# Optimization experiments

Hardware: AMD Instinct MI355X
Metric: run time of the kernel (lower is better)

Reference implementation:

```python
import jax, jax.numpy as jnp
import numpy as np

Nc, Nt, K = 32, 64, 2
P = 1.0
BATCH = 4096
EPS_BIS = 1e-5
MAX_ITER = 100


def setup_inputs() -> dict:
    key = jax.random.key(0)
    ks = jax.random.split(key, 5)
    H = jax.random.normal(ks[0], (BATCH, K, Nc, 2 * Nt), dtype=jnp.float32)
    dims = [2 * K * K, 256, 256, 256, 4 * K]
    inp = {"H": H}
    for i in range(4):
        inp[f"W{i}"] = jax.random.normal(ks[1 + i], (dims[i], dims[i + 1]), dtype=jnp.float32) / float(np.sqrt(dims[i]))
        inp[f"b{i}"] = jnp.zeros((dims[i + 1],), dtype=jnp.float32)
    return inp


def _forward(H, W0, b0, W1, b1, W2, b2, W3, b3):
    batch = H.shape[0]
    eyeK = jnp.eye(K, dtype=jnp.complex64)
    # Source quirk: imag slice H[..., :Nt:2*Nt] has step 2*Nt>Nt -> only column 0, broadcast as imag part
    H1 = H[..., :Nt] + 1j * H[..., 0:Nt:2 * Nt]  # [b,K,Nc,Nt] complex64
    # Analog precoder: conj of center-subcarrier channel per user, unit-modulus normalized
    F_RF = jnp.conj(jnp.transpose(H1[:, :, Nc // 2, :], (0, 2, 1)))  # [b,Nt,K]
    F_RF = F_RF / jnp.abs(F_RF) / np.sqrt(Nt)
    # Source quirk: literal reshape (not permute) mixing batch and subcarrier dims
    H1r = H1.reshape(Nc, batch, K, Nt)
    H_equ = jnp.matmul(H1r, F_RF).reshape(batch, Nc, K, K)  # [Nc,b,K,Nt]@[b,Nt,K] -> [Nc,b,K,K]
    power = jnp.sum(jnp.abs(H_equ) ** 2, axis=(2, 3))  # [b,Nc]
    H_equ = H_equ / jnp.sqrt(power)[:, :, None, None]
    Hf = H_equ.reshape(batch, Nc, K * K)
    x = jnp.concatenate([jnp.real(Hf), jnp.imag(Hf)], axis=2)  # [b,Nc,2*K*K]
    # TRANS_BLOCK stand-in: MLP 8->256->256->256->4K
    for (Wl, bl, act) in ((W0, b0, True), (W1, b1, True), (W2, b2, True), (W3, b3, False)):
        x = x @ Wl + bl
        if act:
            x = jax.nn.relu(x)
    U = (x[..., 0:K] + 1j * x[..., K:2 * K]).astype(jnp.complex64)   # [b,Nc,K]
    Wm = (x[..., 2 * K:3 * K] + 1j * x[..., 3 * K:4 * K]).astype(jnp.complex64)
    Hc = H_equ.astype(jnp.complex64)  # H_hat
    coef = Wm * (jnp.abs(U) ** 2)     # [b,Nc,K]
    # B(mu) = sum_k W_k|U_k|^2 conj(h_k) h_k^T + K*mu*I  (mu*I added K times in source loop)
    B_base = jnp.einsum('bnk,bnki,bnkj->bnij', coef, jnp.conj(Hc), Hc)  # [b,Nc,K,K]
    UW = U * Wm

    def compute_V(mu, Bb, uw, hc):
        Bm = Bb + (K * mu) * eyeK
        Binv = jnp.linalg.inv(Bm)  # batched 2x2 complex inverse
        # V[:,:,i,k] = U_k W_k * (B^{-1} conj(h_k))_i
        return uw[:, :, None, :] * jnp.einsum('bnij,bnkj->bnik', Binv, jnp.conj(hc))

    # Bisection on mu for power constraint sum|V|^2 <= P
    def cond(s):
        lo, hi, mu, it = s
        return jnp.logical_and(hi - lo >= EPS_BIS, it <= MAX_ITER)

    def body(s):
        lo, hi, _, it = s
        mu = (lo + hi) / 2.0
        V = compute_V(mu, B_base, UW, Hc)
        Pitem = jnp.sum(jnp.abs(V) ** 2)
        big = Pitem > P
        return (jnp.where(big, mu, lo), jnp.where(big, hi, mu), mu, it + 1)

    init = (jnp.float32(0.0), jnp.float32(10.0), jnp.float32(5.0), jnp.int32(0))
    _, _, mu, _ = jax.lax.while_loop(cond, body, init)

    V = compute_V(mu, B_base, UW, Hc)  # [b,Nc,K,K]
    F_BB = V.reshape(Nc, batch, K, K)  # literal reshape, as in source
    F_SDMA = jnp.matmul(F_RF, F_BB).reshape(batch, Nc, Nt, K)
    Power = jnp.sum(jnp.abs(F_SDMA) ** 2, axis=(2, 3)).reshape(batch, Nc, 1, 1)
    F_BB = jnp.transpose(F_BB, (1, 0, 2, 3))
    F_BB = F_BB / jnp.sqrt(Power) * np.sqrt(K)
    F_BB = jnp.transpose(F_BB, (1, 0, 2, 3))
    F_SDMA = jnp.matmul(F_RF, F_BB)  # [Nc,b,Nt,K]
    F_SDMA = jnp.transpose(F_SDMA, (1, 0, 2, 3)).reshape(batch, K * Nc * Nt)
    return jnp.concatenate([jnp.real(F_SDMA), jnp.imag(F_SDMA)], axis=1)


def reference(H, W0, b0, W1, b1, W2, b2, W3, b3):
    return _forward(H, W0, b0, W1, b1, W2, b2, W3, b3)
```

## Files before the change

kernel.cpp:

```cpp
#include <hip/hip_runtime.h>

typedef _Float16 f16;
typedef __attribute__((ext_vector_type(8))) _Float16 f16x8;
typedef __attribute__((ext_vector_type(4))) _Float16 f16x4;
typedef __attribute__((ext_vector_type(4))) float f32x4;
typedef unsigned int u32;

#define M2N 131072
#define MFMA16 __builtin_amdgcn_mfma_f32_16x16x32_f16

struct C2 { float x, y; };
__device__ __forceinline__ C2 cmul(C2 a, C2 b){ C2 r; r.x = a.x*b.x - a.y*b.y; r.y = a.x*b.y + a.y*b.x; return r; }
__device__ __forceinline__ C2 cadd(C2 a, C2 b){ C2 r; r.x = a.x+b.x; r.y = a.y+b.y; return r; }
__device__ __forceinline__ C2 csub(C2 a, C2 b){ C2 r; r.x = a.x-b.x; r.y = a.y-b.y; return r; }
__device__ __forceinline__ C2 conjc(C2 a){ C2 r; r.x = a.x; r.y = -a.y; return r; }
__device__ __forceinline__ C2 cneg(C2 a){ C2 r; r.x = -a.x; r.y = -a.y; return r; }
__device__ __forceinline__ float cabs2(C2 a){ return a.x*a.x + a.y*a.y; }
__device__ __forceinline__ float dotr(C2 a, C2 b){ return a.x*b.x + a.y*b.y; }

__device__ __forceinline__ float wred(float v){
  #pragma unroll
  for (int s = 32; s > 0; s >>= 1) v += __shfl_xor(v, s, 64);
  return v;
}

__global__ void k_prep(const float* __restrict__ W0, const float* __restrict__ W1,
                       const float* __restrict__ W2, const float* __restrict__ W3,
                       f16* __restrict__ wfr12, f16* __restrict__ wfr0,
                       f16* __restrict__ wfr3, float* __restrict__ slots)
{
  const int b = blockIdx.x, tid = threadIdx.x;
  if (b < 64){
    const int slot = b*256 + tid;
    const int lane = slot & 63;
    const int rest = slot >> 6;
    const int kt = rest & 7, nt = (rest >> 3) & 15, L = rest >> 7;
    const float* W = L ? W2 : W1;
    const int n = nt*16 + (lane & 15);
    f16* dst = wfr12 + (size_t)rest*1024 + lane*8;
    #pragma unroll
    for (int e = 0; e < 8; ++e){
      const int k = kt*32 + (lane>>4)*8 + e;
      const float w = W[k*256 + n];
      const f16 h = (f16)w;
      dst[e] = h; dst[512+e] = (f16)(w - (float)h);
    }
  } else if (b == 64){
    for (int i = 0; i < 4; ++i){
      const int slot = i*256 + tid;
      const int lane = slot & 63, nt = slot >> 6;
      const int col = nt*16 + (lane & 15);
      f16* dst = wfr0 + (size_t)nt*1024 + lane*8;
      #pragma unroll
      for (int e = 0; e < 8; ++e){
        const int k = (lane>>4)*8 + e;
        const float w = (k < 8) ? W0[k*256 + col] : 0.f;
        const f16 h = (f16)w;
        dst[e] = h; dst[512+e] = (f16)(w - (float)h);
      }
    }
  } else {
    slots[tid] = 0.f;
    for (int i = 0; i < 2; ++i){
      const int slot = i*256 + tid;
      const int lane = slot & 63, kt = slot >> 6;
      const int col = lane & 15;
      f16* dst = wfr3 + (size_t)kt*1024 + lane*8;
      #pragma unroll
      for (int e = 0; e < 8; ++e){
        const int k = kt*32 + (lane>>4)*8 + e;
        const float w = (col < 8) ? W3[k*8 + col] : 0.f;
        const f16 h = (f16)w;
        dst[e] = h; dst[512+e] = (f16)(w - (float)h);
      }
    }
  }
}

__global__ void k_frf(const float* __restrict__ H, float2* __restrict__ frf,
                      float2* __restrict__ g2)
{
  const int b2 = blockIdx.x*2 + (threadIdx.x >> 7);
  const int tt = threadIdx.x & 127;
  const int t = tt >> 1, k = tt & 1;
  __shared__ float2 s[2][128];
  const size_t base = ((size_t)(b2*2 + k)*32 + 16)*128;
  const float are = H[base + t];
  const float aim = H[base];
  const float inv = rsqrtf(are*are + aim*aim) * 0.125f;
  float2 v; v.x = are*inv; v.y = -aim*inv;
  frf[((size_t)b2*64 + t)*2 + k] = v;
  s[threadIdx.x >> 7][tt] = v;
  __syncthreads();
  const int w = threadIdx.x >> 6;
  if ((w & 1) == 0){
    const int half = w >> 1;
    const int lane = threadIdx.x & 63;
    const float2 a = s[half][lane*2];
    const float2 b = s[half][lane*2 + 1];
    float re = a.x*b.x + a.y*b.y;
    float im = a.y*b.x - a.x*b.y;
    re = wred(re); im = wred(im);
    if (lane == 0){ float2 g; g.x = re; g.y = im; g2[blockIdx.x*2 + half] = g; }
  }
}

__global__ void k_hequ(const float* __restrict__ H, const float2* __restrict__ frf,
                       float* __restrict__ x)
{
  const int m2 = blockIdx.x*4 + (threadIdx.x >> 6);
  const int lane = threadIdx.x & 63;
  const int n = m2 >> 12, b2 = m2 & 4095;
  const float4 f = *(const float4*)(frf + ((size_t)b2*64 + lane)*2);
  float accr[2][2], acci[2][2];
  #pragma unroll
  for (int i = 0; i < 2; ++i){
    const float* hr = H + (size_t)(n*8192 + b2*2 + i) * 128;
    const float re = hr[lane];
    const float im = hr[0];
    accr[i][0] = re*f.x - im*f.y;  acci[i][0] = re*f.y + im*f.x;
    accr[i][1] = re*f.z - im*f.w;  acci[i][1] = re*f.w + im*f.z;
  }
  #pragma unroll
  for (int i = 0; i < 2; ++i)
    #pragma unroll
    for (int j = 0; j < 2; ++j){ accr[i][j] = wred(accr[i][j]); acci[i][j] = wred(acci[i][j]); }
  if (lane == 0){
    float pw = 0.f;
    #pragma unroll
    for (int i = 0; i < 2; ++i)
      #pragma unroll
      for (int j = 0; j < 2; ++j) pw += accr[i][j]*accr[i][j] + acci[i][j]*acci[i][j];
    const float rs = rsqrtf(pw);
    *(float4*)(x + (size_t)m2*8)     = make_float4(accr[0][0]*rs, accr[0][1]*rs, accr[1][0]*rs, accr[1][1]*rs);
    *(float4*)(x + (size_t)m2*8 + 4) = make_float4(acci[0][0]*rs, acci[0][1]*rs, acci[1][0]*rs, acci[1][1]*rs);
  }
}

#define SWX(r, c) ((r)*256 + ((c) ^ (((r)&7)<<3)))

__launch_bounds__(256, 3)
__global__ void k_mlp(const float* __restrict__ x, const f16* __restrict__ wfr12,
                      const f16* __restrict__ wfr0, const f16* __restrict__ wfr3,
                      const float* __restrict__ bias0, const float* __restrict__ bias1,
                      const float* __restrict__ bias2, const float* __restrict__ bias3,
                      float* __restrict__ y)
{
  __shared__ __align__(16) f16 xah[48*256];
  __shared__ __align__(16) f16 xal[48*256];
  const int tid = threadIdx.x, blk = blockIdx.x;
  const int lane = tid & 63, wv = tid >> 6;
  const int l15 = lane & 15, lh = lane >> 4;
  const int colb = wv*64;

  f32x4 acc[3][4];
  f16x8 ah[3], al[3], bh[4], bl[4];

  auto EPI = [&](){
    #pragma unroll
    for (int Mt = 0; Mt < 3; ++Mt)
      #pragma unroll
      for (int nt = 0; nt < 4; ++nt){
        f16x4 h4, l4;
        #pragma unroll
        for (int r = 0; r < 4; ++r){
          const float v = fmaxf(acc[Mt][nt][r], 0.f);
          const f16 h = (f16)v;
          h4[r] = h; l4[r] = (f16)(v - (float)h);
        }
        const int idx = SWX(Mt*16 + l15, colb + nt*16 + lh*4);
        *(f16x4*)(xah + idx) = h4;
        *(f16x4*)(xal + idx) = l4;
      }
  };

  #pragma unroll
  for (int nt = 0; nt < 4; ++nt){
    const f32x4 b4 = *(const f32x4*)(bias0 + colb + nt*16 + lh*4);
    #pragma unroll
    for (int Mt = 0; Mt < 3; ++Mt) acc[Mt][nt] = b4;
  }
  #pragma unroll
  for (int Mt = 0; Mt < 3; ++Mt){
    const int row = blk*48 + Mt*16 + l15;
    const float* xr = x + (size_t)row*8;
    const float4 v0 = *(const float4*)xr;
    const float4 v1 = *(const float4*)(xr+4);
    const float vv[8] = {v0.x,v0.y,v0.z,v0.w,v1.x,v1.y,v1.z,v1.w};
    #pragma unroll
    for (int e = 0; e < 8; ++e){
      const f16 h = (f16)vv[e];
      ah[Mt][e] = h; al[Mt][e] = (f16)(vv[e] - (float)h);
    }
  }
  #pragma unroll
  for (int nt = 0; nt < 4; ++nt){
    bh[nt] = *(const f16x8*)(wfr0 + (size_t)(wv*4+nt)*1024 + lane*8);
    bl[nt] = *(const f16x8*)(wfr0 + (size_t)(wv*4+nt)*1024 + 512 + lane*8);
  }
  #pragma unroll
  for (int Mt = 0; Mt < 3; ++Mt)
    #pragma unroll
    for (int nt = 0; nt < 4; ++nt){
      acc[Mt][nt] = MFMA16(bh[nt], ah[Mt], acc[Mt][nt], 0, 0, 0);
      acc[Mt][nt] = MFMA16(bh[nt], al[Mt], acc[Mt][nt], 0, 0, 0);
      acc[Mt][nt] = MFMA16(bl[nt], ah[Mt], acc[Mt][nt], 0, 0, 0);
    }
  EPI();
  __syncthreads();

  for (int L = 0; L < 2; ++L){
    const float* bs = L ? bias2 : bias1;
    #pragma unroll
    for (int nt = 0; nt < 4; ++nt){
      const f32x4 b4 = *(const f32x4*)(bs + colb + nt*16 + lh*4);
      #pragma unroll
      for (int Mt = 0; Mt < 3; ++Mt) acc[Mt][nt] = b4;
    }
    #pragma unroll 2
    for (int kt = 0; kt < 8; ++kt){
      #pragma unroll
      for (int Mt = 0; Mt < 3; ++Mt){
        const int idx = SWX(Mt*16 + l15, kt*32 + lh*8);
        ah[Mt] = *(const f16x8*)(xah + idx);
        al[Mt] = *(const f16x8*)(xal + idx);
      }
      #pragma unroll
      for (int nt = 0; nt < 4; ++nt){
        const size_t f = ((size_t)(L*128 + (wv*4+nt)*8 + kt))*1024;
        bh[nt] = *(const f16x8*)(wfr12 + f + lane*8);
        bl[nt] = *(const f16x8*)(wfr12 + f + 512 + lane*8);
      }
      #pragma unroll
      for (int Mt = 0; Mt < 3; ++Mt)
        #pragma unroll
        for (int nt = 0; nt < 4; ++nt){
          acc[Mt][nt] = MFMA16(bh[nt], ah[Mt], acc[Mt][nt], 0, 0, 0);
          acc[Mt][nt] = MFMA16(bh[nt], al[Mt], acc[Mt][nt], 0, 0, 0);
          acc[Mt][nt] = MFMA16(bl[nt], ah[Mt], acc[Mt][nt], 0, 0, 0);
        }
    }
    __syncthreads();
    EPI();
    __syncthreads();
  }

  f32x4 a3[3];
  {
    f32x4 b4 = {0.f, 0.f, 0.f, 0.f};
    if (lh < 2) b4 = *(const f32x4*)(bias3 + lh*4);
    #pragma unroll
    for (int Mt = 0; Mt < 3; ++Mt) a3[Mt] = b4;
  }
  #pragma unroll 2
  for (int kt = 0; kt < 8; ++kt){
    #pragma unroll
    for (int Mt = 0; Mt < 3; ++Mt){
      const int idx = SWX(Mt*16 + l15, kt*32 + lh*8);
      ah[Mt] = *(const f16x8*)(xah + idx);
      al[Mt] = *(const f16x8*)(xal + idx);
    }
    const f16x8 b3h = *(const f16x8*)(wfr3 + (size_t)kt*1024 + lane*8);
    const f16x8 b3l = *(const f16x8*)(wfr3 + (size_t)kt*1024 + 512 + lane*8);
    #pragma unroll
    for (int Mt = 0; Mt < 3; ++Mt){
      a3[Mt] = MFMA16(b3h, ah[Mt], a3[Mt], 0, 0, 0);
      a3[Mt] = MFMA16(b3h, al[Mt], a3[Mt], 0, 0, 0);
      a3[Mt] = MFMA16(b3l, ah[Mt], a3[Mt], 0, 0, 0);
    }
  }
  if (lh < 2){
    #pragma unroll
    for (int Mt = 0; Mt < 3; ++Mt){
      const int row = blk*48 + Mt*16 + l15;
      if (row < M2N) *(f32x4*)(y + (size_t)row*8 + lh*4) = a3[Mt];
    }
  }
}

struct Elem {
  C2 p[2][2], g[2][2], UW[2], d0, d1;
  float A0, A1, A2, c0, c1, c2, c3;
};
struct Coef { float A0, A1, A2, c0, c1, c2, c3; };

__device__ __forceinline__ void elem_core(const float* __restrict__ x,
                                          const float* __restrict__ y,
                                          int gid, Elem& E)
{
  const float4 xr = *(const float4*)(x + (size_t)gid*8);
  const float4 xi = *(const float4*)(x + (size_t)gid*8 + 4);
  C2 h[2][2];
  h[0][0].x = xr.x; h[0][0].y = xi.x; h[0][1].x = xr.y; h[0][1].y = xi.y;
  h[1][0].x = xr.z; h[1][0].y = xi.z; h[1][1].x = xr.w; h[1][1].y = xi.w;
  const float4 ya = *(const float4*)(y + (size_t)gid*8);
  const float4 yb = *(const float4*)(y + (size_t)gid*8 + 4);
  C2 U[2], Wm[2];
  U[0].x = ya.x; U[0].y = ya.z;  U[1].x = ya.y; U[1].y = ya.w;
  Wm[0].x = yb.x; Wm[0].y = yb.z; Wm[1].x = yb.y; Wm[1].y = yb.w;
  const float u20 = cabs2(U[0]), u21 = cabs2(U[1]);
  C2 cf[2];
  cf[0].x = Wm[0].x*u20; cf[0].y = Wm[0].y*u20;
  cf[1].x = Wm[1].x*u21; cf[1].y = Wm[1].y*u21;
  C2 B[2][2];
  #pragma unroll
  for (int i = 0; i < 2; ++i)
    #pragma unroll
    for (int j = 0; j < 2; ++j){
      const C2 t0 = cmul(conjc(h[0][i]), h[0][j]);
      const C2 t1 = cmul(conjc(h[1][i]), h[1][j]);
      B[i][j] = cadd(cmul(cf[0], t0), cmul(cf[1], t1));
    }
  C2 adj[2][2];
  adj[0][0] = B[1][1]; adj[0][1] = cneg(B[0][1]);
  adj[1][0] = cneg(B[1][0]); adj[1][1] = B[0][0];
  E.d0 = csub(cmul(B[0][0], B[1][1]), cmul(B[0][1], B[1][0]));
  E.d1.x = 2.f*(B[0][0].x + B[1][1].x);
  E.d1.y = 2.f*(B[0][0].y + B[1][1].y);
  #pragma unroll
  for (int k = 0; k < 2; ++k){
    #pragma unroll
    for (int j = 0; j < 2; ++j) E.g[k][j] = conjc(h[k][j]);
    #pragma unroll
    for (int i = 0; i < 2; ++i)
      E.p[k][i] = cadd(cmul(adj[i][0], E.g[k][0]), cmul(adj[i][1], E.g[k][1]));
    E.UW[k] = cmul(U[k], Wm[k]);
  }
  const float w0 = cabs2(E.UW[0]), w1 = cabs2(E.UW[1]);
  E.A0 = w0*(cabs2(E.p[0][0]) + cabs2(E.p[0][1])) + w1*(cabs2(E.p[1][0]) + cabs2(E.p[1][1]));
  E.A1 = 4.f*( w0*(dotr(E.p[0][0], E.g[0][0]) + dotr(E.p[0][1], E.g[0][1]))
             + w1*(dotr(E.p[1][0], E.g[1][0]) + dotr(E.p[1][1], E.g[1][1])) );
  E.A2 = 4.f*( w0*(cabs2(E.g[0][0]) + cabs2(E.g[0][1]))
             + w1*(cabs2(E.g[1][0]) + cabs2(E.g[1][1])) );
  E.c0 = cabs2(E.d0);
  E.c1 = 2.f*(E.d0.x*E.d1.x + E.d0.y*E.d1.y);
  E.c2 = cabs2(E.d1) + 8.f*E.d0.x;
  E.c3 = 8.f*E.d1.x;
}

__device__ __forceinline__ float evalf(float mu, const Coef& C){
  const float num = C.A0 + mu*(C.A1 + mu*C.A2);
  const float den = C.c0 + mu*(C.c1 + mu*(C.c2 + mu*(C.c3 + mu*16.f)));
  return num/den;
}

__device__ __forceinline__ void replay(const float* __restrict__ slots, int nrounds,
                                       float& lo, float& hi)
{
  const int DP[4] = {5, 5, 5, 4};
  for (int r = 0; r < nrounds; ++r){
    const float lo0 = lo, span = hi - lo;
    int k = 0;
    for (int d = 0; d < DP[r]; ++d){
      const float sd = span * (1.0f / (float)(1 << (d+1)));
      const float mu = fmaf((float)(2*k + 1), sd, lo0);
      const bool big = slots[r*32 + (1 << d) - 1 + k] > 1.0f;
      lo = big ? mu : lo;
      hi = big ? hi : mu;
      k = 2*k + (big ? 1 : 0);
    }
  }
}

__global__ void k_coef(const float* __restrict__ x, const float* __restrict__ y,
                       float* __restrict__ coef)
{
  const int gid = blockIdx.x*256 + threadIdx.x;
  Elem E;
  elem_core(x, y, gid, E);
  *(float4*)(coef + (size_t)gid*8)     = make_float4(E.A0, E.A1, E.A2, E.c0);
  *(float4*)(coef + (size_t)gid*8 + 4) = make_float4(E.c1, E.c2, E.c3, 0.f);
}

template<int ROUND, int D>
__global__ void k_red(const float* __restrict__ coef, float* __restrict__ slots)
{
  const int tid = threadIdx.x;
  const int gid = blockIdx.x*256 + tid;
  const int lane = tid & 63, wv = tid >> 6;
  __shared__ float r4[4][32];

  const float4 a = *(const float4*)(coef + (size_t)gid*8);
  const float4 b = *(const float4*)(coef + (size_t)gid*8 + 4);
  Coef C; C.A0 = a.x; C.A1 = a.y; C.A2 = a.z; C.c0 = a.w;
  C.c1 = b.x; C.c2 = b.y; C.c3 = b.z;

  float lo = 0.f, hi = 10.f;
  replay(slots, ROUND, lo, hi);

  const float lo0 = lo, span = hi - lo;
  int node = 0;
  #pragma unroll
  for (int d = 0; d < D; ++d){
    const float sd = span * (1.0f / (float)(1 << (d+1)));
    for (int k = 0; k < (1 << d); ++k){
      const float mu = fmaf((float)(2*k + 1), sd, lo0);
      const float f = wred(evalf(mu, C));
      if (lane == 0) r4[wv][node] = f;
      ++node;
    }
  }
  __syncthreads();
  if (tid < (1 << D) - 1)
    atomicAdd(&slots[ROUND*32 + tid], r4[0][tid] + r4[1][tid] + r4[2][tid] + r4[3][tid]);
}

__global__ void k_final(const float* __restrict__ x, const float* __restrict__ y,
                        const float2* __restrict__ g2, const float* __restrict__ slots,
                        float2* __restrict__ V, float* __restrict__ Pm)
{
  const int gid = blockIdx.x*256 + threadIdx.x;
  float lo = 0.f, hi = 10.f;
  replay(slots, 4, lo, hi);
  const float mu = 0.5f*(lo + hi);

  Elem E;
  elem_core(x, y, gid, E);
  C2 det; det.x = E.d0.x + mu*E.d1.x + 4.f*mu*mu; det.y = E.d0.y + mu*E.d1.y;
  const float id = 1.f/cabs2(det);
  C2 idet; idet.x = det.x*id; idet.y = -det.y*id;
  C2 Vv[2][2];
  #pragma unroll
  for (int k = 0; k < 2; ++k)
    #pragma unroll
    for (int i = 0; i < 2; ++i){
      C2 t; t.x = E.p[k][i].x + 2.f*mu*E.g[k][i].x; t.y = E.p[k][i].y + 2.f*mu*E.g[k][i].y;
      Vv[i][k] = cmul(E.UW[k], cmul(t, idet));
    }
  *(float4*)(V + (size_t)gid*4)     = make_float4(Vv[0][0].x, Vv[0][0].y, Vv[0][1].x, Vv[0][1].y);
  *(float4*)(V + (size_t)gid*4 + 2) = make_float4(Vv[1][0].x, Vv[1][0].y, Vv[1][1].x, Vv[1][1].y);
  const float2 gg2 = g2[gid & 4095];
  C2 gc; gc.x = gg2.x; gc.y = gg2.y;
  float P = 0.f;
  #pragma unroll
  for (int k = 0; k < 2; ++k){
    const C2 a = Vv[0][k], b = Vv[1][k];
    P += cabs2(a) + cabs2(b);
    const C2 t = cmul(gc, cmul(a, conjc(b)));
    P += 2.f*t.x;
  }
  Pm[gid] = P;
}

__global__ void k_out(const float2* __restrict__ frf, const float2* __restrict__ V,
                      const float* __restrict__ Pm, float* __restrict__ out)
{
  const int b2 = blockIdx.x;
  const int t = threadIdx.x & 63;
  const int ng = threadIdx.x >> 6;
  const float4 f = *(const float4*)(frf + ((size_t)b2*64 + t)*2);
  C2 f0, f1; f0.x = f.x; f0.y = f.y; f1.x = f.z; f1.y = f.w;
  for (int n = ng; n < 32; n += 4){
    const float4* mv = (const float4*)(V + ((size_t)n*4096 + b2)*4);
    const float4 m0 = mv[0];
    const float4 m1 = mv[1];
    C2 M00, M01, M10, M11;
    M00.x = m0.x; M00.y = m0.y; M01.x = m0.z; M01.y = m0.w;
    M10.x = m1.x; M10.y = m1.y; M11.x = m1.z; M11.y = m1.w;
    const float sc = 1.41421356237f * rsqrtf(Pm[b2*32 + n]);
    const C2 c0 = cadd(cmul(f0, M00), cmul(f1, M10));
    const C2 c1 = cadd(cmul(f0, M01), cmul(f1, M11));
    const size_t base = (size_t)b2*8192 + n*128 + t*2;
    *(float2*)(out + base)        = make_float2(c0.x*sc, c1.x*sc);
    *(float2*)(out + base + 4096) = make_float2(c0.y*sc, c1.y*sc);
  }
}

extern "C" void kernel_launch(void* const* d_in, const int* in_sizes, int n_in,
                              void* d_out, int out_size, void* d_ws, size_t ws_size,
                              hipStream_t stream)
{
  const float* H  = (const float*)d_in[0];
  const float* W0 = (const float*)d_in[1];
  const float* b0 = (const float*)d_in[2];
  const float* W1 = (const float*)d_in[3];
  const float* b1 = (const float*)d_in[4];
  const float* W2 = (const float*)d_in[5];
  const float* b2 = (const float*)d_in[6];
  const float* W3 = (const float*)d_in[7];
  const float* b3 = (const float*)d_in[8];
  float* out = (float*)d_out;
  char* ws = (char*)d_ws;
  (void)in_sizes; (void)n_in; (void)out_size; (void)ws_size;

  size_t o = 0;
  auto alloc = [&](size_t bytes) -> void* {
    void* p = ws + o;
    o += (bytes + 255) & ~(size_t)255;
    return p;
  };
  float2* frf   = (float2*)alloc((size_t)4096*64*2*sizeof(float2));
  float2* g2    = (float2*)alloc((size_t)4096*sizeof(float2));
  float*  xbuf  = (float*) alloc((size_t)M2N*8*sizeof(float));
  float*  ybuf  = (float*) alloc((size_t)M2N*8*sizeof(float));
  float2* V     = (float2*)alloc((size_t)M2N*4*sizeof(float2));
  float*  Pm    = (float*) alloc((size_t)M2N*sizeof(float));
  float*  coef  = (float*) alloc((size_t)M2N*8*sizeof(float));
  float*  slots = (float*) alloc(256*sizeof(float));
  f16*    wfr12 = (f16*)   alloc((size_t)256*1024*sizeof(f16));
  f16*    wfr0  = (f16*)   alloc((size_t)16*1024*sizeof(f16));
  f16*    wfr3  = (f16*)   alloc((size_t)8*1024*sizeof(f16));

  k_prep<<<66, 256, 0, stream>>>(W0, W1, W2, W3, wfr12, wfr0, wfr3, slots);
  k_frf<<<2048, 256, 0, stream>>>(H, frf, g2);
  k_hequ<<<32768, 256, 0, stream>>>(H, frf, xbuf);
  k_mlp<<<2731, 256, 0, stream>>>(xbuf, wfr12, wfr0, wfr3, b0, b1, b2, b3, ybuf);
  k_coef<<<512, 256, 0, stream>>>(xbuf, ybuf, coef);
  k_red<0,5><<<512, 256, 0, stream>>>(coef, slots);
  k_red<1,5><<<512, 256, 0, stream>>>(coef, slots);
  k_red<2,5><<<512, 256, 0, stream>>>(coef, slots);
  k_red<3,4><<<512, 256, 0, stream>>>(coef, slots);
  k_final<<<512, 256, 0, stream>>>(xbuf, ybuf, g2, slots, V, Pm);
  k_out<<<4096, 256, 0, stream>>>(frf, V, Pm, out);
}
```

Before: 274.5 us.

## Fuse coef into MLP epilogue, fuse final V into output, double-buffer MLP weights

The per-element bisection coefficients are now computed in the MLP kernel's epilogue from the layer-3 output staged in shared memory, which removes the separate k_coef kernel. V and the power normalisation are computed inside k_out, so k_final and the V/Pm global buffers go away. The MLP K-loops are also restructured to double-buffer weight fragment loads so the next tile's global loads overlap the MFMAs. The trade-offs are more register pressure in k_mlp, and in k_out each element's V is computed twice (once for V, once for the power term) plus a block barrier.

New measurement: 286.5 us. 1.04x slower.

```diff
diff --git a/kernel.cpp b/kernel.cpp
--- a/kernel.cpp
+++ b/kernel.cpp
@@ -137,6 +137,69 @@
   }
 }
 
+struct Elem {
+  C2 p[2][2], g[2][2], UW[2], d0, d1;
+  float A0, A1, A2, c0, c1, c2, c3;
+};
+struct Coef { float A0, A1, A2, c0, c1, c2, c3; };
+
+__device__ __forceinline__ void elem_core_v(float4 xr, float4 xi, float4 ya, float4 yb,
+                                            Elem& E)
+{
+  C2 h[2][2];
+  h[0][0].x = xr.x; h[0][0].y = xi.x; h[0][1].x = xr.y; h[0][1].y = xi.y;
+  h[1][0].x = xr.z; h[1][0].y = xi.z; h[1][1].x = xr.w; h[1][1].y = xi.w;
+  C2 U[2], Wm[2];
+  U[0].x = ya.x; U[0].y = ya.z;  U[1].x = ya.y; U[1].y = ya.w;
+  Wm[0].x = yb.x; Wm[0].y = yb.z; Wm[1].x = yb.y; Wm[1].y = yb.w;
+  const float u20 = cabs2(U[0]), u21 = cabs2(U[1]);
+  C2 cf[2];
+  cf[0].x = Wm[0].x*u20; cf[0].y = Wm[0].y*u20;
+  cf[1].x = Wm[1].x*u21; cf[1].y = Wm[1].y*u21;
+  C2 B[2][2];
+  #pragma unroll
+  for (int i = 0; i < 2; ++i)
+    #pragma unroll
+    for (int j = 0; j < 2; ++j){
+      const C2 t0 = cmul(conjc(h[0][i]), h[0][j]);
+      const C2 t1 = cmul(conjc(h[1][i]), h[1][j]);
+      B[i][j] = cadd(cmul(cf[0], t0), cmul(cf[1], t1));
+    }
+  C2 adj[2][2];
+  adj[0][0] = B[1][1]; adj[0][1] = cneg(B[0][1]);
+  adj[1][0] = cneg(B[1][0]); adj[1][1] = B[0][0];
+  E.d0 = csub(cmul(B[0][0], B[1][1]), cmul(B[0][1], B[1][0]));
+  E.d1.x = 2.f*(B[0][0].x + B[1][1].x);
+  E.d1.y = 2.f*(B[0][0].y + B[1][1].y);
+  #pragma unroll
+  for (int k = 0; k < 2; ++k){
+    #pragma unroll
+    for (int j = 0; j < 2; ++j) E.g[k][j] = conjc(h[k][j]);
+    #pragma unroll
+    for (int i = 0; i < 2; ++i)
+      E.p[k][i] = cadd(cmul(adj[i][0], E.g[k][0]), cmul(adj[i][1], E.g[k][1]));
+    E.UW[k] = cmul(U[k], Wm[k]);
+  }
+  const float w0 = cabs2(E.UW[0]), w1 = cabs2(E.UW[1]);
+  E.A0 = w0*(cabs2(E.p[0][0]) + cabs2(E.p[0][1])) + w1*(cabs2(E.p[1][0]) + cabs2(E.p[1][1]));
+  E.A1 = 4.f*( w0*(dotr(E.p[0][0], E.g[0][0]) + dotr(E.p[0][1], E.g[0][1]))
+             + w1*(dotr(E.p[1][0], E.g[1][0]) + dotr(E.p[1][1], E.g[1][1])) );
+  E.A2 = 4.f*( w0*(cabs2(E.g[0][0]) + cabs2(E.g[0][1]))
+             + w1*(cabs2(E.g[1][0]) + cabs2(E.g[1][1])) );
+  E.c0 = cabs2(E.d0);
+  E.c1 = 2.f*(E.d0.x*E.d1.x + E.d0.y*E.d1.y);
+  E.c2 = cabs2(E.d1) + 8.f*E.d0.x;
+  E.c3 = 8.f*E.d1.x;
+}
+
+__device__ __forceinline__ void elem_core(const float* __restrict__ x,
+                                          const float* __restrict__ y,
+                                          int gid, Elem& E)
+{
+  elem_core_v(*(const float4*)(x + (size_t)gid*8), *(const float4*)(x + (size_t)gid*8 + 4),
+              *(const float4*)(y + (size_t)gid*8), *(const float4*)(y + (size_t)gid*8 + 4), E);
+}
+
 #define SWX(r, c) ((r)*256 + ((c) ^ (((r)&7)<<3)))
 
 __launch_bounds__(256, 3)
@@ -144,7 +207,7 @@
                       const f16* __restrict__ wfr0, const f16* __restrict__ wfr3,
                       const float* __restrict__ bias0, const float* __restrict__ bias1,
                       const float* __restrict__ bias2, const float* __restrict__ bias3,
-                      float* __restrict__ y)
+                      float* __restrict__ y, float* __restrict__ coef)
 {
   __shared__ __align__(16) f16 xah[48*256];
   __shared__ __align__(16) f16 xal[48*256];
@@ -154,7 +217,7 @@
   const int colb = wv*64;
 
   f32x4 acc[3][4];
-  f16x8 ah[3], al[3], bh[4], bl[4];
+  f16x8 ah[3], al[3];
 
   auto EPI = [&](){
     #pragma unroll
@@ -173,72 +236,109 @@
         *(f16x4*)(xal + idx) = l4;
       }
   };
-
-  #pragma unroll
-  for (int nt = 0; nt < 4; ++nt){
-    const f32x4 b4 = *(const f32x4*)(bias0 + colb + nt*16 + lh*4);
-    #pragma unroll
-    for (int Mt = 0; Mt < 3; ++Mt) acc[Mt][nt] = b4;
-  }
-  #pragma unroll
-  for (int Mt = 0; Mt < 3; ++Mt){
-    const int row = blk*48 + Mt*16 + l15;
-    const float* xr = x + (size_t)row*8;
-    const float4 v0 = *(const float4*)xr;
-    const float4 v1 = *(const float4*)(xr+4);
-    const float vv[8] = {v0.x,v0.y,v0.z,v0.w,v1.x,v1.y,v1.z,v1.w};
-    #pragma unroll
-    for (int e = 0; e < 8; ++e){
-      const f16 h = (f16)vv[e];
-      ah[Mt][e] = h; al[Mt][e] = (f16)(vv[e] - (float)h);
-    }
-  }
-  #pragma unroll
-  for (int nt = 0; nt < 4; ++nt){
-    bh[nt] = *(const f16x8*)(wfr0 + (size_t)(wv*4+nt)*1024 + lane*8);
-    bl[nt] = *(const f16x8*)(wfr0 + (size_t)(wv*4+nt)*1024 + 512 + lane*8);
-  }
-  #pragma unroll
-  for (int Mt = 0; Mt < 3; ++Mt)
+  auto LDA = [&](int kt){
+    #pragma unroll
+    for (int Mt = 0; Mt < 3; ++Mt){
+      const int idx = SWX(Mt*16 + l15, kt*32 + lh*8);
+      ah[Mt] = *(const f16x8*)(xah + idx);
+      al[Mt] = *(const f16x8*)(xal + idx);
+    }
+  };
+
+  {
+    f16x8 bh[4], bl[4];
     #pragma unroll
     for (int nt = 0; nt < 4; ++nt){
-      acc[Mt][nt] = MFMA16(bh[nt], ah[Mt], acc[Mt][nt], 0, 0, 0);
-      acc[Mt][nt] = MFMA16(bh[nt], al[Mt], acc[Mt][nt], 0, 0, 0);
-      acc[Mt][nt] = MFMA16(bl[nt], ah[Mt], acc[Mt][nt], 0, 0, 0);
-    }
-  EPI();
+      const f32x4 b4 = *(const f32x4*)(bias0 + colb + nt*16 + lh*4);
+      #pragma unroll
+      for (int Mt = 0; Mt < 3; ++Mt) acc[Mt][nt] = b4;
+    }
+    #pragma unroll
+    for (int Mt = 0; Mt < 3; ++Mt){
+      const int row = blk*48 + Mt*16 + l15;
+      const float* xr = x + (size_t)row*8;
+      const float4 v0 = *(const float4*)xr;
+      const float4 v1 = *(const float4*)(xr+4);
+      const float vv[8] = {v0.x,v0.y,v0.z,v0.w,v1.x,v1.y,v1.z,v1.w};
+      #pragma unroll
+      for (int e = 0; e < 8; ++e){
+        const f16 h = (f16)vv[e];
+        ah[Mt][e] = h; al[Mt][e] = (f16)(vv[e] - (float)h);
+      }
+    }
+    #pragma unroll
+    for (int nt = 0; nt < 4; ++nt){
+      bh[nt] = *(const f16x8*)(wfr0 + (size_t)(wv*4+nt)*1024 + lane*8);
+      bl[nt] = *(const f16x8*)(wfr0 + (size_t)(wv*4+nt)*1024 + 512 + lane*8);
+    }
+    #pragma unroll
+    for (int Mt = 0; Mt < 3; ++Mt)
+      #pragma unroll
+      for (int nt = 0; nt < 4; ++nt){
+        acc[Mt][nt] = MFMA16(bh[nt], ah[Mt], acc[Mt][nt], 0, 0, 0);
+        acc[Mt][nt] = MFMA16(bh[nt], al[Mt], acc[Mt][nt], 0, 0, 0);
+        acc[Mt][nt] = MFMA16(bl[nt], ah[Mt], acc[Mt][nt], 0, 0, 0);
+      }
+    EPI();
+  }
   __syncthreads();
 
   for (int L = 0; L < 2; ++L){
     const float* bs = L ? bias2 : bias1;
+    const f16* wL = wfr12 + (size_t)L*131072;
     #pragma unroll
     for (int nt = 0; nt < 4; ++nt){
       const f32x4 b4 = *(const f32x4*)(bs + colb + nt*16 + lh*4);
       #pragma unroll
       for (int Mt = 0; Mt < 3; ++Mt) acc[Mt][nt] = b4;
     }
-    #pragma unroll 2
-    for (int kt = 0; kt < 8; ++kt){
-      #pragma unroll
-      for (int Mt = 0; Mt < 3; ++Mt){
-        const int idx = SWX(Mt*16 + l15, kt*32 + lh*8);
-        ah[Mt] = *(const f16x8*)(xah + idx);
-        al[Mt] = *(const f16x8*)(xal + idx);
-      }
+    f16x8 b0h[4], b0l[4], b1h[4], b1l[4];
+    auto LDB0 = [&](int kt){
       #pragma unroll
       for (int nt = 0; nt < 4; ++nt){
-        const size_t f = ((size_t)(L*128 + (wv*4+nt)*8 + kt))*1024;
-        bh[nt] = *(const f16x8*)(wfr12 + f + lane*8);
-        bl[nt] = *(const f16x8*)(wfr12 + f + 512 + lane*8);
-      }
+        const size_t f = ((size_t)((wv*4+nt)*8 + kt))*1024;
+        b0h[nt] = *(const f16x8*)(wL + f + lane*8);
+        b0l[nt] = *(const f16x8*)(wL + f + 512 + lane*8);
+      }
+    };
+    auto LDB1 = [&](int kt){
+      #pragma unroll
+      for (int nt = 0; nt < 4; ++nt){
+        const size_t f = ((size_t)((wv*4+nt)*8 + kt))*1024;
+        b1h[nt] = *(const f16x8*)(wL + f + lane*8);
+        b1l[nt] = *(const f16x8*)(wL + f + 512 + lane*8);
+      }
+    };
+    auto FMA0 = [&](){
       #pragma unroll
       for (int Mt = 0; Mt < 3; ++Mt)
         #pragma unroll
         for (int nt = 0; nt < 4; ++nt){
-          acc[Mt][nt] = MFMA16(bh[nt], ah[Mt], acc[Mt][nt], 0, 0, 0);
-          acc[Mt][nt] = MFMA16(bh[nt], al[Mt], acc[Mt][nt], 0, 0, 0);
-          acc[Mt][nt] = MFMA16(bl[nt], ah[Mt], acc[Mt][nt], 0, 0, 0);
+          acc[Mt][nt] = MFMA16(b0h[nt], ah[Mt], acc[Mt][nt], 0, 0, 0);
+          acc[Mt][nt] = MFMA16(b0h[nt], al[Mt], acc[Mt][nt], 0, 0, 0);
+          acc[Mt][nt] = MFMA16(b0l[nt], ah[Mt], acc[Mt][nt], 0, 0, 0);
         }
+    };
+    auto FMA1 = [&](){
+      #pragma unroll
+      for (int Mt = 0; Mt < 3; ++Mt)
+        #pragma unroll
+        for (int nt = 0; nt < 4; ++nt){
+          acc[Mt][nt] = MFMA16(b1h[nt], ah[Mt], acc[Mt][nt], 0, 0, 0);
+          acc[Mt][nt] = MFMA16(b1h[nt], al[Mt], acc[Mt][nt], 0, 0, 0);
+          acc[Mt][nt] = MFMA16(b1l[nt], ah[Mt], acc[Mt][nt], 0, 0, 0);
+        }
+    };
+    LDB0(0);
+    #pragma unroll
+    for (int kp = 0; kp < 4; ++kp){
+      const int kt = kp*2;
+      LDB1(kt + 1);
+      LDA(kt);
+      FMA0();
+      if (kt + 2 < 8) LDB0(kt + 2);
+      LDA(kt + 1);
+      FMA1();
     }
     __syncthreads();
     EPI();
@@ -252,21 +352,33 @@
     #pragma unroll
     for (int Mt = 0; Mt < 3; ++Mt) a3[Mt] = b4;
   }
-  #pragma unroll 2
-  for (int kt = 0; kt < 8; ++kt){
-    #pragma unroll
-    for (int Mt = 0; Mt < 3; ++Mt){
-      const int idx = SWX(Mt*16 + l15, kt*32 + lh*8);
-      ah[Mt] = *(const f16x8*)(xah + idx);
-      al[Mt] = *(const f16x8*)(xal + idx);
-    }
-    const f16x8 b3h = *(const f16x8*)(wfr3 + (size_t)kt*1024 + lane*8);
-    const f16x8 b3l = *(const f16x8*)(wfr3 + (size_t)kt*1024 + 512 + lane*8);
-    #pragma unroll
-    for (int Mt = 0; Mt < 3; ++Mt){
-      a3[Mt] = MFMA16(b3h, ah[Mt], a3[Mt], 0, 0, 0);
-      a3[Mt] = MFMA16(b3h, al[Mt], a3[Mt], 0, 0, 0);
-      a3[Mt] = MFMA16(b3l, ah[Mt], a3[Mt], 0, 0, 0);
+  {
+    f16x8 c0h, c0l, c1h, c1l;
+    c0h = *(const f16x8*)(wfr3 + lane*8);
+    c0l = *(const f16x8*)(wfr3 + 512 + lane*8);
+    #pragma unroll
+    for (int kp = 0; kp < 4; ++kp){
+      const int kt = kp*2;
+      c1h = *(const f16x8*)(wfr3 + (size_t)(kt+1)*1024 + lane*8);
+      c1l = *(const f16x8*)(wfr3 + (size_t)(kt+1)*1024 + 512 + lane*8);
+      LDA(kt);
+      #pragma unroll
+      for (int Mt = 0; Mt < 3; ++Mt){
+        a3[Mt] = MFMA16(c0h, ah[Mt], a3[Mt], 0, 0, 0);
+        a3[Mt] = MFMA16(c0h, al[Mt], a3[Mt], 0, 0, 0);
+        a3[Mt] = MFMA16(c0l, ah[Mt], a3[Mt], 0, 0, 0);
+      }
+      if (kt + 2 < 8){
+        c0h = *(const f16x8*)(wfr3 + (size_t)(kt+2)*1024 + lane*8);
+        c0l = *(const f16x8*)(wfr3 + (size_t)(kt+2)*1024 + 512 + lane*8);
+      }
+      LDA(kt + 1);
+      #pragma unroll
+      for (int Mt = 0; Mt < 3; ++Mt){
+        a3[Mt] = MFMA16(c1h, ah[Mt], a3[Mt], 0, 0, 0);
+        a3[Mt] = MFMA16(c1h, al[Mt], a3[Mt], 0, 0, 0);
+        a3[Mt] = MFMA16(c1l, ah[Mt], a3[Mt], 0, 0, 0);
+      }
     }
   }
   if (lh < 2){
@@ -276,66 +388,31 @@
       if (row < M2N) *(f32x4*)(y + (size_t)row*8 + lh*4) = a3[Mt];
     }
   }
-}
-
-struct Elem {
-  C2 p[2][2], g[2][2], UW[2], d0, d1;
-  float A0, A1, A2, c0, c1, c2, c3;
-};
-struct Coef { float A0, A1, A2, c0, c1, c2, c3; };
-
-__device__ __forceinline__ void elem_core(const float* __restrict__ x,
-                                          const float* __restrict__ y,
-                                          int gid, Elem& E)
-{
-  const float4 xr = *(const float4*)(x + (size_t)gid*8);
-  const float4 xi = *(const float4*)(x + (size_t)gid*8 + 4);
-  C2 h[2][2];
-  h[0][0].x = xr.x; h[0][0].y = xi.x; h[0][1].x = xr.y; h[0][1].y = xi.y;
-  h[1][0].x = xr.z; h[1][0].y = xi.z; h[1][1].x = xr.w; h[1][1].y = xi.w;
-  const float4 ya = *(const float4*)(y + (size_t)gid*8);
-  const float4 yb = *(const float4*)(y + (size_t)gid*8 + 4);
-  C2 U[2], Wm[2];
-  U[0].x = ya.x; U[0].y = ya.z;  U[1].x = ya.y; U[1].y = ya.w;
-  Wm[0].x = yb.x; Wm[0].y = yb.z; Wm[1].x = yb.y; Wm[1].y = yb.w;
-  const float u20 = cabs2(U[0]), u21 = cabs2(U[1]);
-  C2 cf[2];
-  cf[0].x = Wm[0].x*u20; cf[0].y = Wm[0].y*u20;
-  cf[1].x = Wm[1].x*u21; cf[1].y = Wm[1].y*u21;
-  C2 B[2][2];
-  #pragma unroll
-  for (int i = 0; i < 2; ++i)
-    #pragma unroll
-    for (int j = 0; j < 2; ++j){
-      const C2 t0 = cmul(conjc(h[0][i]), h[0][j]);
-      const C2 t1 = cmul(conjc(h[1][i]), h[1][j]);
-      B[i][j] = cadd(cmul(cf[0], t0), cmul(cf[1], t1));
-    }
-  C2 adj[2][2];
-  adj[0][0] = B[1][1]; adj[0][1] = cneg(B[0][1]);
-  adj[1][0] = cneg(B[1][0]); adj[1][1] = B[0][0];
-  E.d0 = csub(cmul(B[0][0], B[1][1]), cmul(B[0][1], B[1][0]));
-  E.d1.x = 2.f*(B[0][0].x + B[1][1].x);
-  E.d1.y = 2.f*(B[0][0].y + B[1][1].y);
-  #pragma unroll
-  for (int k = 0; k < 2; ++k){
-    #pragma unroll
-    for (int j = 0; j < 2; ++j) E.g[k][j] = conjc(h[k][j]);
-    #pragma unroll
-    for (int i = 0; i < 2; ++i)
-      E.p[k][i] = cadd(cmul(adj[i][0], E.g[k][0]), cmul(adj[i][1], E.g[k][1]));
-    E.UW[k] = cmul(U[k], Wm[k]);
-  }
-  const float w0 = cabs2(E.UW[0]), w1 = cabs2(E.UW[1]);
-  E.A0 = w0*(cabs2(E.p[0][0]) + cabs2(E.p[0][1])) + w1*(cabs2(E.p[1][0]) + cabs2(E.p[1][1]));
-  E.A1 = 4.f*( w0*(dotr(E.p[0][0], E.g[0][0]) + dotr(E.p[0][1], E.g[0][1]))
-             + w1*(dotr(E.p[1][0], E.g[1][0]) + dotr(E.p[1][1], E.g[1][1])) );
-  E.A2 = 4.f*( w0*(cabs2(E.g[0][0]) + cabs2(E.g[0][1]))
-             + w1*(cabs2(E.g[1][0]) + cabs2(E.g[1][1])) );
-  E.c0 = cabs2(E.d0);
-  E.c1 = 2.f*(E.d0.x*E.d1.x + E.d0.y*E.d1.y);
-  E.c2 = cabs2(E.d1) + 8.f*E.d0.x;
-  E.c3 = 8.f*E.d1.x;
+
+  __syncthreads();
+  {
+    float* yl = (float*)xal;
+    if (lh < 2){
+      #pragma unroll
+      for (int Mt = 0; Mt < 3; ++Mt)
+        *(f32x4*)(yl + (Mt*16 + l15)*8 + lh*4) = a3[Mt];
+    }
+  }
+  __syncthreads();
+  if (tid < 48){
+    const int row = blk*48 + tid;
+    if (row < M2N){
+      const float* yl = (const float*)xal;
+      const float4 xr = *(const float4*)(x + (size_t)row*8);
+      const float4 xi = *(const float4*)(x + (size_t)row*8 + 4);
+      const float4 ya = *(const float4*)(yl + tid*8);
+      const float4 yb = *(const float4*)(yl + tid*8 + 4);
+      Elem E;
+      elem_core_v(xr, xi, ya, yb, E);
+      *(float4*)(coef + (size_t)row*8)     = make_float4(E.A0, E.A1, E.A2, E.c0);
+      *(float4*)(coef + (size_t)row*8 + 4) = make_float4(E.c1, E.c2, E.c3, 0.f);
+    }
+  }
 }
 
 __device__ __forceinline__ float evalf(float mu, const Coef& C){
@@ -362,16 +439,6 @@
   }
 }
 
-__global__ void k_coef(const float* __restrict__ x, const float* __restrict__ y,
-                       float* __restrict__ coef)
-{
-  const int gid = blockIdx.x*256 + threadIdx.x;
-  Elem E;
-  elem_core(x, y, gid, E);
-  *(float4*)(coef + (size_t)gid*8)     = make_float4(E.A0, E.A1, E.A2, E.c0);
-  *(float4*)(coef + (size_t)gid*8 + 4) = make_float4(E.c1, E.c2, E.c3, 0.f);
-}
-
 template<int ROUND, int D>
 __global__ void k_red(const float* __restrict__ coef, float* __restrict__ slots)
 {
@@ -405,59 +472,65 @@
     atomicAdd(&slots[ROUND*32 + tid], r4[0][tid] + r4[1][tid] + r4[2][tid] + r4[3][tid]);
 }
 
-__global__ void k_final(const float* __restrict__ x, const float* __restrict__ y,
-                        const float2* __restrict__ g2, const float* __restrict__ slots,
-                        float2* __restrict__ V, float* __restrict__ Pm)
-{
-  const int gid = blockIdx.x*256 + threadIdx.x;
-  float lo = 0.f, hi = 10.f;
-  replay(slots, 4, lo, hi);
-  const float mu = 0.5f*(lo + hi);
-
-  Elem E;
-  elem_core(x, y, gid, E);
-  C2 det; det.x = E.d0.x + mu*E.d1.x + 4.f*mu*mu; det.y = E.d0.y + mu*E.d1.y;
-  const float id = 1.f/cabs2(det);
-  C2 idet; idet.x = det.x*id; idet.y = -det.y*id;
-  C2 Vv[2][2];
-  #pragma unroll
-  for (int k = 0; k < 2; ++k)
-    #pragma unroll
-    for (int i = 0; i < 2; ++i){
-      C2 t; t.x = E.p[k][i].x + 2.f*mu*E.g[k][i].x; t.y = E.p[k][i].y + 2.f*mu*E.g[k][i].y;
-      Vv[i][k] = cmul(E.UW[k], cmul(t, idet));
-    }
-  *(float4*)(V + (size_t)gid*4)     = make_float4(Vv[0][0].x, Vv[0][0].y, Vv[0][1].x, Vv[0][1].y);
-  *(float4*)(V + (size_t)gid*4 + 2) = make_float4(Vv[1][0].x, Vv[1][0].y, Vv[1][1].x, Vv[1][1].y);
-  const float2 gg2 = g2[gid & 4095];
-  C2 gc; gc.x = gg2.x; gc.y = gg2.y;
-  float P = 0.f;
-  #pragma unroll
-  for (int k = 0; k < 2; ++k){
-    const C2 a = Vv[0][k], b = Vv[1][k];
-    P += cabs2(a) + cabs2(b);
-    const C2 t = cmul(gc, cmul(a, conjc(b)));
-    P += 2.f*t.x;
-  }
-  Pm[gid] = P;
-}
-
-__global__ void k_out(const float2* __restrict__ frf, const float2* __restrict__ V,
-                      const float* __restrict__ Pm, float* __restrict__ out)
+__global__ void k_out(const float2* __restrict__ frf, const float* __restrict__ x,
+                      const float* __restrict__ y, const float2* __restrict__ g2,
+                      const float* __restrict__ slots, float* __restrict__ out)
 {
   const int b2 = blockIdx.x;
-  const int t = threadIdx.x & 63;
-  const int ng = threadIdx.x >> 6;
+  const int tid = threadIdx.x;
+  __shared__ float Vs[32][8];
+  __shared__ float scs[32];
+
+  if (tid < 64){
+    const int n = tid & 31;
+    const bool isP = tid >= 32;
+    const int gid = isP ? (b2*32 + n) : (n*4096 + b2);
+    float lo = 0.f, hi = 10.f;
+    replay(slots, 4, lo, hi);
+    const float mu = 0.5f*(lo + hi);
+    Elem E;
+    elem_core(x, y, gid, E);
+    C2 det; det.x = E.d0.x + mu*E.d1.x + 4.f*mu*mu; det.y = E.d0.y + mu*E.d1.y;
+    const float id = 1.f/cabs2(det);
+    C2 idet; idet.x = det.x*id; idet.y = -det.y*id;
+    C2 Vv[2][2];
+    #pragma unroll
+    for (int k = 0; k < 2; ++k)
+      #pragma unroll
+      for (int i = 0; i < 2; ++i){
+        C2 t; t.x = E.p[k][i].x + 2.f*mu*E.g[k][i].x; t.y = E.p[k][i].y + 2.f*mu*E.g[k][i].y;
+        Vv[i][k] = cmul(E.UW[k], cmul(t, idet));
+      }
+    if (!isP){
+      Vs[n][0] = Vv[0][0].x; Vs[n][1] = Vv[0][0].y;
+      Vs[n][2] = Vv[0][1].x; Vs[n][3] = Vv[0][1].y;
+      Vs[n][4] = Vv[1][0].x; Vs[n][5] = Vv[1][0].y;
+      Vs[n][6] = Vv[1][1].x; Vs[n][7] = Vv[1][1].y;
+    } else {
+      const float2 gg2 = g2[gid & 4095];
+      C2 gc; gc.x = gg2.x; gc.y = gg2.y;
+      float P = 0.f;
+      #pragma unroll
+      for (int k = 0; k < 2; ++k){
+        const C2 a = Vv[0][k], b = Vv[1][k];
+        P += cabs2(a) + cabs2(b);
+        const C2 t = cmul(gc, cmul(a, conjc(b)));
+        P += 2.f*t.x;
+      }
+      scs[n] = 1.41421356237f * rsqrtf(P);
+    }
+  }
+  __syncthreads();
+
+  const int t = tid & 63;
+  const int ng = tid >> 6;
   const float4 f = *(const float4*)(frf + ((size_t)b2*64 + t)*2);
   C2 f0, f1; f0.x = f.x; f0.y = f.y; f1.x = f.z; f1.y = f.w;
   for (int n = ng; n < 32; n += 4){
-    const float4* mv = (const float4*)(V + ((size_t)n*4096 + b2)*4);
-    const float4 m0 = mv[0];
-    const float4 m1 = mv[1];
     C2 M00, M01, M10, M11;
-    M00.x = m0.x; M00.y = m0.y; M01.x = m0.z; M01.y = m0.w;
-    M10.x = m1.x; M10.y = m1.y; M11.x = m1.z; M11.y = m1.w;
-    const float sc = 1.41421356237f * rsqrtf(Pm[b2*32 + n]);
+    M00.x = Vs[n][0]; M00.y = Vs[n][1]; M01.x = Vs[n][2]; M01.y = Vs[n][3];
+    M10.x = Vs[n][4]; M10.y = Vs[n][5]; M11.x = Vs[n][6]; M11.y = Vs[n][7];
+    const float sc = scs[n];
     const C2 c0 = cadd(cmul(f0, M00), cmul(f1, M10));
     const C2 c1 = cadd(cmul(f0, M01), cmul(f1, M11));
     const size_t base = (size_t)b2*8192 + n*128 + t*2;
@@ -493,8 +566,6 @@
   float2* g2    = (float2*)alloc((size_t)4096*sizeof(float2));
   float*  xbuf  = (float*) alloc((size_t)M2N*8*sizeof(float));
   float*  ybuf  = (float*) alloc((size_t)M2N*8*sizeof(float));
-  float2* V     = (float2*)alloc((size_t)M2N*4*sizeof(float2));
-  float*  Pm    = (float*) alloc((size_t)M2N*sizeof(float));
   float*  coef  = (float*) alloc((size_t)M2N*8*sizeof(float));
   float*  slots = (float*) alloc(256*sizeof(float));
   f16*    wfr12 = (f16*)   alloc((size_t)256*1024*sizeof(f16));
@@ -504,12 +575,10 @@
   k_prep<<<66, 256, 0, stream>>>(W0, W1, W2, W3, wfr12, wfr0, wfr3, slots);
   k_frf<<<2048, 256, 0, stream>>>(H, frf, g2);
   k_hequ<<<32768, 256, 0, stream>>>(H, frf, xbuf);
-  k_mlp<<<2731, 256, 0, stream>>>(xbuf, wfr12, wfr0, wfr3, b0, b1, b2, b3, ybuf);
-  k_coef<<<512, 256, 0, stream>>>(xbuf, ybuf, coef);
+  k_mlp<<<2731, 256, 0, stream>>>(xbuf, wfr12, wfr0, wfr3, b0, b1, b2, b3, ybuf, coef);
   k_red<0,5><<<512, 256, 0, stream>>>(coef, slots);
   k_red<1,5><<<512, 256, 0, stream>>>(coef, slots);
   k_red<2,5><<<512, 256, 0, stream>>>(coef, slots);
   k_red<3,4><<<512, 256, 0, stream>>>(coef, slots);
-  k_final<<<512, 256, 0, stream>>>(xbuf, ybuf, g2, slots, V, Pm);
-  k_out<<<4096, 256, 0, stream>>>(frf, V, Pm, out);
-}
+  k_out<<<4096, 256, 0, stream>>>(frf, xbuf, ybuf, g2, slots, out);
+}
```
